# Kernel tuning notes

Measured on AMD Instinct MI355X. Metric: run time of the kernel, lower is better.

Reference implementation:

```python
import jax, jax.numpy as jnp
import numpy as np

S, B, E, H = 2048, 2, 1024, 16
D = E // H  # head_dim = 64


def setup_inputs() -> dict:
    key = jax.random.key(0)
    ks = jax.random.split(key, 5)
    sp = (2.0 / (E + E)) ** 0.5  # xavier-ish scale
    return {
        "x": jax.random.normal(ks[0], (S, B, E), dtype=jnp.float32),
        "wq": jax.random.normal(ks[1], (E, E), dtype=jnp.float32) * sp,
        "bq": jnp.zeros((E,), jnp.float32),
        "wk": jax.random.normal(ks[2], (E, E), dtype=jnp.float32) * sp,
        "bk": jnp.zeros((E,), jnp.float32),
        "wv": jax.random.normal(ks[3], (E, E), dtype=jnp.float32) * sp,
        "bv": jnp.zeros((E,), jnp.float32),
        "wo": jax.random.normal(ks[4], (E, E), dtype=jnp.float32) * sp,
        "bo": jnp.zeros((E,), jnp.float32),
    }


def reference(x, wq, bq, wk, bk, wv, bv, wo, bo):
    # x: (S, B, E), weights in torch Linear convention (out, in)
    scaling = jnp.float32(D ** -0.5)
    q = (jnp.einsum('ibe,fe->ibf', x, wq) + bq) * scaling
    k = jnp.einsum('ibe,fe->ibf', x, wk) + bk
    v = jnp.einsum('ibe,fe->ibf', x, wv) + bv
    q = q.reshape(S, B, H, D)
    k = k.reshape(S, B, H, D)
    v = v.reshape(S, B, H, D)
    # energy: (B, H, S_q, S_k)
    energy = jnp.einsum('ibnf,jbnf->bnij', q, k)
    causal = jnp.triu(jnp.ones((S, S), dtype=bool), k=1)  # True above diagonal
    energy = jnp.where(causal[None, None], -jnp.inf, energy)
    weights = jax.nn.softmax(energy, axis=-1)
    head_ctx = jnp.einsum('bnij,jbnf->ibnf', weights, v)
    context = head_ctx.reshape(S, B, E)
    out = jnp.einsum('ibe,fe->ibf', context, wo) + bo
    return out
```

## Files before the change

kernel.cpp:

```cpp
#include <hip/hip_runtime.h>
#include <hip/hip_bf16.h>
#include <stdint.h>

#define S_LEN 2048
#define BATCH 2
#define EMB   1024
#define NH    16
#define HD    64
#define LOG2E 1.4426950408889634f

typedef __bf16 bf16x8 __attribute__((ext_vector_type(8)));
typedef float  f32x4  __attribute__((ext_vector_type(4)));
typedef unsigned short ushort8 __attribute__((ext_vector_type(8)));

__device__ __forceinline__ unsigned short f2bf(float f) {
  __bf16 h = (__bf16)f;
  return __builtin_bit_cast(unsigned short, h);
}

__device__ __forceinline__ ushort8 cvt8(const float4 a, const float4 b) {
  ushort8 o;
  o[0]=f2bf(a.x); o[1]=f2bf(a.y); o[2]=f2bf(a.z); o[3]=f2bf(a.w);
  o[4]=f2bf(b.x); o[5]=f2bf(b.y); o[6]=f2bf(b.z); o[7]=f2bf(b.w);
  return o;
}

__device__ __forceinline__ uint2 pack4(const f32x4 v) {
  uint2 r;
  r.x = (unsigned)f2bf(v[0]) | ((unsigned)f2bf(v[1]) << 16);
  r.y = (unsigned)f2bf(v[2]) | ((unsigned)f2bf(v[3]) << 16);
  return r;
}

#define GLOAD16(g, l) __builtin_amdgcn_global_load_lds( \
    (const __attribute__((address_space(1))) void*)(g),  \
    (__attribute__((address_space(3))) void*)(l), 16, 0, 0)

__global__ __launch_bounds__(256) void k_cvt(const float* __restrict__ src,
                                             unsigned short* __restrict__ dst,
                                             int n) {
  int i = (blockIdx.x*256 + threadIdx.x)*8;
  if (i >= n) return;
  const float4* s4 = (const float4*)(src + i);
  *(ushort8*)(dst + i) = cvt8(s4[0], s4[1]);
}

__global__ __launch_bounds__(256) void k_cvt_all(
    const float* __restrict__ x,
    const float* __restrict__ wq, const float* __restrict__ wk,
    const float* __restrict__ wv, const float* __restrict__ wo,
    unsigned short* __restrict__ xb, unsigned short* __restrict__ wb,
    unsigned short* __restrict__ wob) {
  const int b = blockIdx.x;
  const float* src;
  unsigned short* dst;
  int off;
  if (b < 2048) { src = x; dst = xb; off = b; }
  else {
    const int t = b - 2048;
    const int z = t >> 9;
    if (z < 3) { src = (z==0) ? wq : ((z==1) ? wk : wv); dst = wb + (size_t)z*EMB*EMB; }
    else       { src = wo; dst = wob; }
    off = t & 511;
  }
  const int i = (off*256 + threadIdx.x)*8;
  const float4* s4 = (const float4*)(src + i);
  *(ushort8*)(dst + i) = cvt8(s4[0], s4[1]);
}

__global__ __launch_bounds__(256) void k_qkv_bb(
    const unsigned short* __restrict__ xb,
    const unsigned short* __restrict__ wb,
    const float* __restrict__ bq, const float* __restrict__ bk,
    const float* __restrict__ bv,
    unsigned short* __restrict__ Qb, unsigned short* __restrict__ Kb,
    unsigned short* __restrict__ Vtb)
{
  __shared__ unsigned short Al[2][128*32];
  __shared__ unsigned short Bl[2][128*32];
  const int tid = threadIdx.x;
  const int lin  = blockIdx.x;
  const int wgid = (lin & 7)*96 + (lin >> 3);
  const int mb   = wgid / 24;
  const int t    = wgid % 24;
  const int z    = t >> 3;
  const int nb   = t & 7;
  const int m0 = mb * 128;
  const int n0 = nb * 128;
  const int w = tid >> 6, lane = tid & 63;
  const int wr = w >> 1, wc = w & 1;
  const int lr = lane & 15, lhi = lane >> 4;
  const unsigned short* wz = wb + (size_t)z * (EMB*EMB);

  const unsigned short* ag[2];
  const unsigned short* bg[2];
  int ub[2];
#pragma unroll
  for (int j=0;j<2;++j) {
    const int c   = j*256 + tid;
    const int row = c >> 2;
    const int col = (c & 3) << 3;
    ag[j] = xb + (size_t)(m0+row)*EMB + col;
    bg[j] = wz + (size_t)(n0+row)*EMB + col;
    ub[j] = (j*256 + (tid & 192)) * 16;
  }

  auto STAGE = [&](int k0, int b2) {
#pragma unroll
    for (int j=0;j<2;++j) {
      GLOAD16(ag[j] + k0, (char*)Al[b2] + ub[j]);
      GLOAD16(bg[j] + k0, (char*)Bl[b2] + ub[j]);
    }
  };

  f32x4 acc[4][4];
#pragma unroll
  for (int m=0;m<4;++m)
#pragma unroll
    for (int n=0;n<4;++n) acc[m][n] = (f32x4){0.f,0.f,0.f,0.f};

  STAGE(0, 0);
  int bbuf = 0;
  for (int k0 = 0; k0 < EMB; k0 += 32) {
    if (k0 + 32 < EMB) {
      STAGE(k0 + 32, bbuf^1);
      asm volatile("s_waitcnt vmcnt(4)" ::: "memory");
    } else {
      asm volatile("s_waitcnt vmcnt(0)" ::: "memory");
    }
    __builtin_amdgcn_s_barrier();

    bf16x8 af[4], bfr[4];
#pragma unroll
    for (int m=0;m<4;++m) af[m]  = *(const bf16x8*)&Al[bbuf][(wr*64 + m*16 + lr)*32 + lhi*8];
#pragma unroll
    for (int n=0;n<4;++n) bfr[n] = *(const bf16x8*)&Bl[bbuf][(wc*64 + n*16 + lr)*32 + lhi*8];
    __builtin_amdgcn_s_setprio(1);
#pragma unroll
    for (int m=0;m<4;++m)
#pragma unroll
      for (int n=0;n<4;++n)
        acc[m][n] = __builtin_amdgcn_mfma_f32_16x16x32_bf16(af[m], bfr[n], acc[m][n], 0,0,0);
    __builtin_amdgcn_s_setprio(0);

    __builtin_amdgcn_s_barrier();
    bbuf ^= 1;
  }

  const float scale = (z==0) ? 0.125f*LOG2E : 1.0f;
  const float* bias = (z==0) ? bq : ((z==1) ? bk : bv);
#pragma unroll
  for (int m=0;m<4;++m)
#pragma unroll
    for (int n=0;n<4;++n)
#pragma unroll
      for (int r=0;r<4;++r) {
        const int rr   = m0 + wr*64 + m*16 + lhi*4 + r;
        const int fcol = n0 + wc*64 + n*16 + lr;
        const float v = (acc[m][n][r] + bias[fcol]) * scale;
        const unsigned short ov = f2bf(v);
        const int i = rr >> 1, bsel = rr & 1;
        const int h = fcol >> 6, d = fcol & 63;
        const int hh = bsel*NH + h;
        if (z == 0)      Qb [((size_t)hh*S_LEN + i)*HD + d] = ov;
        else if (z == 1) Kb [((size_t)hh*S_LEN + i)*HD + d] = ov;
        else             Vtb[((size_t)hh*HD + d)*S_LEN + i] = ov;
      }
}

__global__ __launch_bounds__(256) void k_qkv_bf(
    const unsigned short* __restrict__ xb,
    const float* __restrict__ wq, const float* __restrict__ wk,
    const float* __restrict__ wv,
    const float* __restrict__ bq, const float* __restrict__ bk,
    const float* __restrict__ bv,
    unsigned short* __restrict__ Qb, unsigned short* __restrict__ Kb,
    unsigned short* __restrict__ Vtb)
{
  __shared__ unsigned short Al[128*32];
  __shared__ unsigned short Bl[128*32];
  const int tid = threadIdx.x;
  const int lin  = blockIdx.x;
  const int wgid = (lin & 7)*96 + (lin >> 3);
  const int mb   = wgid / 24;
  const int t    = wgid % 24;
  const int z    = t >> 3;
  const int nb   = t & 7;
  const int m0 = mb * 128;
  const int n0 = nb * 128;
  const int w = tid >> 6, lane = tid & 63;
  const int wr = w >> 1, wc = w & 1;
  const int lr = lane & 15, lhi = lane >> 4;
  const float* wz = (z==0) ? wq : ((z==1) ? wk : wv);

  f32x4 acc[4][4];
#pragma unroll
  for (int m=0;m<4;++m)
#pragma unroll
    for (int n=0;n<4;++n) acc[m][n] = (f32x4){0.f,0.f,0.f,0.f};

  for (int k0 = 0; k0 < EMB; k0 += 32) {
    float4 b0[2], b1[2];
#pragma unroll
    for (int j = 0; j < 2; ++j) {
      const int c   = j*256 + tid;
      const int row = c >> 2;
      const int col = (c & 3) << 3;
      const float* bp = wz + (size_t)(n0+row)*EMB + k0 + col;
      b0[j] = *(const float4*)bp;  b1[j] = *(const float4*)(bp+4);
    }
    __syncthreads();
#pragma unroll
    for (int j = 0; j < 2; ++j) {
      const int c   = j*256 + tid;
      const int row = c >> 2;
      const int col = (c & 3) << 3;
      const int ub  = (j*256 + (tid & 192)) * 16;
      GLOAD16(xb + (size_t)(m0+row)*EMB + k0 + col, (char*)Al + ub);
      *(ushort8*)&Bl[row*32 + col] = cvt8(b0[j], b1[j]);
    }
    __syncthreads();
    bf16x8 af[4], bfr[4];
#pragma unroll
    for (int m=0;m<4;++m) af[m]  = *(const bf16x8*)&Al[(wr*64 + m*16 + lr)*32 + lhi*8];
#pragma unroll
    for (int n=0;n<4;++n) bfr[n] = *(const bf16x8*)&Bl[(wc*64 + n*16 + lr)*32 + lhi*8];
#pragma unroll
    for (int m=0;m<4;++m)
#pragma unroll
      for (int n=0;n<4;++n)
        acc[m][n] = __builtin_amdgcn_mfma_f32_16x16x32_bf16(af[m], bfr[n], acc[m][n], 0,0,0);
  }

  const float scale = (z==0) ? 0.125f*LOG2E : 1.0f;
  const float* bias = (z==0) ? bq : ((z==1) ? bk : bv);
#pragma unroll
  for (int m=0;m<4;++m)
#pragma unroll
    for (int n=0;n<4;++n)
#pragma unroll
      for (int r=0;r<4;++r) {
        const int rr   = m0 + wr*64 + m*16 + lhi*4 + r;
        const int fcol = n0 + wc*64 + n*16 + lr;
        const float v = (acc[m][n][r] + bias[fcol]) * scale;
        const unsigned short ov = f2bf(v);
        const int i = rr >> 1, bsel = rr & 1;
        const int h = fcol >> 6, d = fcol & 63;
        const int hh = bsel*NH + h;
        if (z == 0)      Qb [((size_t)hh*S_LEN + i)*HD + d] = ov;
        else if (z == 1) Kb [((size_t)hh*S_LEN + i)*HD + d] = ov;
        else             Vtb[((size_t)hh*HD + d)*S_LEN + i] = ov;
      }
}

__global__ __launch_bounds__(256) void k_qkv(
    const float* __restrict__ xA, int a_rs, int ishift,
    const float* __restrict__ wq, const float* __restrict__ wk,
    const float* __restrict__ wv,
    const float* __restrict__ bq, const float* __restrict__ bk,
    const float* __restrict__ bv,
    unsigned short* __restrict__ Qb, unsigned short* __restrict__ Kb,
    unsigned short* __restrict__ Vtb)
{
  __shared__ unsigned short Al[128*32];
  __shared__ unsigned short Bl[128*32];
  const int tid = threadIdx.x;
  const int z  = blockIdx.z;
  const int m0 = blockIdx.x * 128;
  const int n0 = blockIdx.y * 128;
  const int w = tid >> 6, lane = tid & 63;
  const int wr = w >> 1, wc = w & 1;
  const int lr = lane & 15, lhi = lane >> 4;
  const float* wz = (z==0) ? wq : ((z==1) ? wk : wv);

  f32x4 acc[4][4];
#pragma unroll
  for (int m=0;m<4;++m)
#pragma unroll
    for (int n=0;n<4;++n) acc[m][n] = (f32x4){0.f,0.f,0.f,0.f};

  for (int k0 = 0; k0 < EMB; k0 += 32) {
    float4 a0[2], a1[2], b0[2], b1[2];
#pragma unroll
    for (int j = 0; j < 2; ++j) {
      const int c   = j*256 + tid;
      const int row = c >> 2;
      const int col = (c & 3) << 3;
      const float* ap = xA + (size_t)(m0+row)*a_rs + k0 + col;
      const float* bp = wz + (size_t)(n0+row)*EMB + k0 + col;
      a0[j] = *(const float4*)ap;  a1[j] = *(const float4*)(ap+4);
      b0[j] = *(const float4*)bp;  b1[j] = *(const float4*)(bp+4);
    }
    __syncthreads();
#pragma unroll
    for (int j = 0; j < 2; ++j) {
      const int c   = j*256 + tid;
      const int row = c >> 2;
      const int col = (c & 3) << 3;
      *(ushort8*)&Al[row*32 + col] = cvt8(a0[j], a1[j]);
      *(ushort8*)&Bl[row*32 + col] = cvt8(b0[j], b1[j]);
    }
    __syncthreads();
    bf16x8 af[4], bfr[4];
#pragma unroll
    for (int m=0;m<4;++m) af[m]  = *(const bf16x8*)&Al[(wr*64 + m*16 + lr)*32 + lhi*8];
#pragma unroll
    for (int n=0;n<4;++n) bfr[n] = *(const bf16x8*)&Bl[(wc*64 + n*16 + lr)*32 + lhi*8];
#pragma unroll
    for (int m=0;m<4;++m)
#pragma unroll
      for (int n=0;n<4;++n)
        acc[m][n] = __builtin_amdgcn_mfma_f32_16x16x32_bf16(af[m], bfr[n], acc[m][n], 0,0,0);
  }

  const float scale = (z==0) ? 0.125f*LOG2E : 1.0f;
  const float* bias = (z==0) ? bq : ((z==1) ? bk : bv);
  const int bmask = (1 << ishift) - 1;
#pragma unroll
  for (int m=0;m<4;++m)
#pragma unroll
    for (int n=0;n<4;++n)
#pragma unroll
      for (int r=0;r<4;++r) {
        const int rr   = m0 + wr*64 + m*16 + lhi*4 + r;
        const int fcol = n0 + wc*64 + n*16 + lr;
        const float v = (acc[m][n][r] + bias[fcol]) * scale;
        const unsigned short ov = f2bf(v);
        const int i = rr >> ishift, bsel = rr & bmask;
        const int h = fcol >> 6, d = fcol & 63;
        const int hh = bsel*NH + h;
        if (z == 0)      Qb [((size_t)hh*S_LEN + i)*HD + d] = ov;
        else if (z == 1) Kb [((size_t)hh*S_LEN + i)*HD + d] = ov;
        else             Vtb[((size_t)hh*HD + d)*S_LEN + i] = ov;
      }
}

__global__ __launch_bounds__(256,4) void k_attn_u(
    const unsigned short* __restrict__ Q,
    const unsigned short* __restrict__ K,
    const unsigned short* __restrict__ Vt,
    unsigned short* __restrict__ ctx, int bshift, int hsh)
{
  __shared__ unsigned short KL[2][64*64];
  __shared__ unsigned short VL[2][64*64];
  __shared__ unsigned short Pl[4][16*64];

  const int tid = threadIdx.x;
  const int w = tid >> 6, lane = tid & 63;
  const int lr = lane & 15, lhi = lane >> 4;

  const int lin = blockIdx.x;
  const int cc  = lin >> hsh;
  const int chunk = (cc < 16) ? cc : (47 - cc);
  const int hh  = lin & ((1 << hsh) - 1);
  const int q0  = chunk*64 + w*16;

  const unsigned short* Qh = Q  + (size_t)hh*S_LEN*HD;
  const unsigned short* Kh = K  + (size_t)hh*S_LEN*HD;
  const unsigned short* Vh = Vt + (size_t)hh*HD*S_LEN;
  char* Pw = (char*)Pl[w];

  const int xm = (lr & 7) << 4;
  int kvb[2];
#pragma unroll
  for (int kf=0;kf<2;++kf) kvb[kf] = lr*128 + ((kf*64 + lhi*16) ^ xm);
  int pwb[4];
#pragma unroll
  for (int kn=0;kn<4;++kn)
    pwb[kn] = lr*128 + ((kn*32 + lhi*8) ^ xm);

  const unsigned short* kga[2];
  const unsigned short* vga[2];
#pragma unroll
  for (int j=0;j<2;++j) {
    const int c   = j*256 + tid;
    const int row = c >> 3;
    const int sb  = (c*16) ^ ((row & 7) << 4);
    const int el  = (sb & 127) >> 1;
    kga[j] = Kh + (size_t)row*HD + el;
    vga[j] = Vh + (size_t)row*S_LEN + el;
  }
  const int ub0 = (tid & 192) * 16;

  bf16x8 qf[2];
#pragma unroll
  for (int kf=0;kf<2;++kf)
    qf[kf] = *(const bf16x8*)&Qh[(size_t)(q0 + lr)*HD + kf*32 + lhi*8];

  f32x4 o[4];
  float rl = 0.f;
#pragma unroll
  for (int dn=0;dn<4;++dn) o[dn] = (f32x4){0.f,0.f,0.f,0.f};

  const int tmax = chunk + 1;

  auto STAGE = [&](int tt, int bb2) {
#pragma unroll
    for (int j=0;j<2;++j) {
      GLOAD16(kga[j] + (size_t)tt*4096, (char*)KL[bb2] + ub0 + j*4096);
      GLOAD16(vga[j] + (size_t)tt*64,   (char*)VL[bb2] + ub0 + j*4096);
    }
  };

  STAGE(0, 0);
  int bb = 0;
  for (int t = 0; t < tmax; ++t) {
    if (t + 1 < tmax) {
      STAGE(t+1, bb^1);
      asm volatile("s_waitcnt vmcnt(4)" ::: "memory");
    } else {
      asm volatile("s_waitcnt vmcnt(0)" ::: "memory");
    }
    __builtin_amdgcn_s_barrier();

    const int kv0 = t*64;
    const char* KB = (const char*)KL[bb];
    const char* VB = (const char*)VL[bb];

    f32x4 st[4];
#pragma unroll
    for (int kn=0;kn<4;++kn) st[kn] = (f32x4){0.f,0.f,0.f,0.f};

    __builtin_amdgcn_s_setprio(1);
#pragma unroll
    for (int kn=0;kn<4;++kn)
#pragma unroll
      for (int kf=0;kf<2;++kf) {
        const bf16x8 kfr = *(const bf16x8*)(KB + kvb[kf] + kn*2048);
        st[kn] = __builtin_amdgcn_mfma_f32_16x16x32_bf16(kfr, qf[kf], st[kn], 0,0,0);
      }
    __builtin_amdgcn_s_setprio(0);

    if (t == tmax-1) {
      const int q = q0 + lr;
#pragma unroll
      for (int kn=0;kn<4;++kn)
#pragma unroll
        for (int r=0;r<4;++r) {
          const int k = kv0 + kn*16 + lhi*4 + r;
          if (k > q) st[kn][r] = -1.0e30f;
        }
    }

#pragma unroll
    for (int kn=0;kn<4;++kn)
#pragma unroll
      for (int r=0;r<4;++r) {
        const float p = exp2f(st[kn][r]);
        st[kn][r] = p;
        rl += p;
      }

#pragma unroll
    for (int kn=0;kn<4;++kn)
      *(uint2*)(Pw + pwb[kn]) = pack4(st[kn]);

#pragma unroll
    for (int ks=0;ks<2;++ks) {
      const bf16x8 pfr = *(const bf16x8*)(Pw + kvb[ks]);
      __builtin_amdgcn_s_setprio(1);
#pragma unroll
      for (int dn=0;dn<4;++dn) {
        const bf16x8 vf = *(const bf16x8*)(VB + kvb[ks] + dn*2048);
        o[dn] = __builtin_amdgcn_mfma_f32_16x16x32_bf16(vf, pfr, o[dn], 0,0,0);
      }
      __builtin_amdgcn_s_setprio(0);
    }

    __builtin_amdgcn_s_barrier();
    bb ^= 1;
  }

  rl += __shfl_xor(rl, 16);
  rl += __shfl_xor(rl, 32);
  const int h = hh & (NH-1);
  const int badd = hh >> 4;
  const float inv = 1.0f / rl;
  const int q = q0 + lr;
  const size_t trow = ((size_t)q << bshift) + badd;
#pragma unroll
  for (int dn=0;dn<4;++dn) {
    f32x4 ov;
#pragma unroll
    for (int r=0;r<4;++r) ov[r] = o[dn][r]*inv;
    *(uint2*)&ctx[trow*EMB + h*HD + dn*16 + lhi*4] = pack4(ov);
  }
}

__global__ __launch_bounds__(256) void k_oproj_bf(
    const unsigned short* __restrict__ ctxA,
    const unsigned short* __restrict__ wob,
    const float* __restrict__ bo,
    float* __restrict__ out)
{
  __shared__ unsigned short Al[2][128*32];
  __shared__ unsigned short Bl[2][128*32];
  const int tid = threadIdx.x;
  const int m0 = blockIdx.x * 128;
  const int n0 = blockIdx.y * 128;
  const int w = tid >> 6, lane = tid & 63;
  const int wr = w >> 1, wc = w & 1;
  const int lr = lane & 15, lhi = lane >> 4;

  const unsigned short* ag[2];
  const unsigned short* bg[2];
  int ub[2];
#pragma unroll
  for (int j=0;j<2;++j) {
    const int c   = j*256 + tid;
    const int row = c >> 2;
    const int col = (c & 3) << 3;
    ag[j] = ctxA + (size_t)(m0+row)*EMB + col;
    bg[j] = wob  + (size_t)(n0+row)*EMB + col;
    ub[j] = (j*256 + (tid & 192)) * 16;
  }

  auto STAGE = [&](int k0, int b2) {
#pragma unroll
    for (int j=0;j<2;++j) {
      GLOAD16(ag[j] + k0, (char*)Al[b2] + ub[j]);
      GLOAD16(bg[j] + k0, (char*)Bl[b2] + ub[j]);
    }
  };

  f32x4 acc[4][4];
#pragma unroll
  for (int m=0;m<4;++m)
#pragma unroll
    for (int n=0;n<4;++n) acc[m][n] = (f32x4){0.f,0.f,0.f,0.f};

  STAGE(0, 0);
  int bbuf = 0;
  for (int k0 = 0; k0 < EMB; k0 += 32) {
    if (k0 + 32 < EMB) {
      STAGE(k0 + 32, bbuf^1);
      asm volatile("s_waitcnt vmcnt(4)" ::: "memory");
    } else {
      asm volatile("s_waitcnt vmcnt(0)" ::: "memory");
    }
    __builtin_amdgcn_s_barrier();

    bf16x8 af[4], bfr[4];
#pragma unroll
    for (int m=0;m<4;++m) af[m]  = *(const bf16x8*)&Al[bbuf][(wr*64 + m*16 + lr)*32 + lhi*8];
#pragma unroll
    for (int n=0;n<4;++n) bfr[n] = *(const bf16x8*)&Bl[bbuf][(wc*64 + n*16 + lr)*32 + lhi*8];
    __builtin_amdgcn_s_setprio(1);
#pragma unroll
    for (int m=0;m<4;++m)
#pragma unroll
      for (int n=0;n<4;++n)
        acc[m][n] = __builtin_amdgcn_mfma_f32_16x16x32_bf16(af[m], bfr[n], acc[m][n], 0,0,0);
    __builtin_amdgcn_s_setprio(0);

    __builtin_amdgcn_s_barrier();
    bbuf ^= 1;
  }

#pragma unroll
  for (int m=0;m<4;++m)
#pragma unroll
    for (int n=0;n<4;++n)
#pragma unroll
      for (int r=0;r<4;++r) {
        const int rr   = m0 + wr*64 + m*16 + lhi*4 + r;
        const int fcol = n0 + wc*64 + n*16 + lr;
        out[(size_t)rr*EMB + fcol] = acc[m][n][r] + bo[fcol];
      }
}

__global__ __launch_bounds__(256) void k_oproj(
    const unsigned short* __restrict__ ctxA,
    const float* __restrict__ wo,
    const float* __restrict__ bo,
    float* __restrict__ outb, int orm)
{
  __shared__ unsigned short Al[128*32];
  __shared__ unsigned short Bl[128*32];
  const int tid = threadIdx.x;
  const int m0 = blockIdx.x * 128;
  const int n0 = blockIdx.y * 128;
  const int w = tid >> 6, lane = tid & 63;
  const int wr = w >> 1, wc = w & 1;
  const int lr = lane & 15, lhi = lane >> 4;

  f32x4 acc[4][4];
#pragma unroll
  for (int m=0;m<4;++m)
#pragma unroll
    for (int n=0;n<4;++n) acc[m][n] = (f32x4){0.f,0.f,0.f,0.f};

  for (int k0 = 0; k0 < EMB; k0 += 32) {
    float4 b0[2], b1[2];
#pragma unroll
    for (int j = 0; j < 2; ++j) {
      const int c   = j*256 + tid;
      const int row = c >> 2;
      const int col = (c & 3) << 3;
      const float* bp = wo + (size_t)(n0+row)*EMB + k0 + col;
      b0[j] = *(const float4*)bp;  b1[j] = *(const float4*)(bp+4);
    }
    __syncthreads();
#pragma unroll
    for (int j = 0; j < 2; ++j) {
      const int c   = j*256 + tid;
      const int row = c >> 2;
      const int col = (c & 3) << 3;
      const int ub  = (j*256 + (tid & 192)) * 16;
      GLOAD16(ctxA + (size_t)(m0+row)*EMB + k0 + col, (char*)Al + ub);
      *(ushort8*)&Bl[row*32 + col] = cvt8(b0[j], b1[j]);
    }
    __syncthreads();
    bf16x8 af[4], bfr[4];
#pragma unroll
    for (int m=0;m<4;++m) af[m]  = *(const bf16x8*)&Al[(wr*64 + m*16 + lr)*32 + lhi*8];
#pragma unroll
    for (int n=0;n<4;++n) bfr[n] = *(const bf16x8*)&Bl[(wc*64 + n*16 + lr)*32 + lhi*8];
#pragma unroll
    for (int m=0;m<4;++m)
#pragma unroll
      for (int n=0;n<4;++n)
        acc[m][n] = __builtin_amdgcn_mfma_f32_16x16x32_bf16(af[m], bfr[n], acc[m][n], 0,0,0);
  }

#pragma unroll
  for (int m=0;m<4;++m)
#pragma unroll
    for (int n=0;n<4;++n)
#pragma unroll
      for (int r=0;r<4;++r) {
        const int rr   = m0 + wr*64 + m*16 + lhi*4 + r;
        const int fcol = n0 + wc*64 + n*16 + lr;
        outb[(size_t)rr*orm*EMB + fcol] = acc[m][n][r] + bo[fcol];
      }
}

extern "C" void kernel_launch(void* const* d_in, const int* in_sizes, int n_in,
                              void* d_out, int out_size, void* d_ws, size_t ws_size,
                              hipStream_t stream) {
  const float* x  = (const float*)d_in[0];
  const float* wq = (const float*)d_in[1];
  const float* bq = (const float*)d_in[2];
  const float* wk = (const float*)d_in[3];
  const float* bk = (const float*)d_in[4];
  const float* wv = (const float*)d_in[5];
  const float* bv = (const float*)d_in[6];
  const float* wo = (const float*)d_in[7];
  const float* bo = (const float*)d_in[8];
  float* out = (float*)d_out;

  char* ws = (char*)d_ws;
  const size_t MB = (size_t)1 << 20;

  if (ws_size >= 40*MB) {
    unsigned short* Q   = (unsigned short*)(ws + 0*MB);
    unsigned short* K   = (unsigned short*)(ws + 8*MB);
    unsigned short* Vt  = (unsigned short*)(ws + 16*MB);
    unsigned short* wb  = (unsigned short*)(ws + 24*MB);
    unsigned short* xb  = (unsigned short*)(ws + 30*MB);
    unsigned short* wob = (unsigned short*)(ws + 38*MB);
    unsigned short* cx  = (unsigned short*)(ws + 24*MB);

    k_cvt_all<<<4096, 256, 0, stream>>>(x, wq, wk, wv, wo, xb, wb, wob);
    k_qkv_bb<<<768, 256, 0, stream>>>(xb, wb, bq,bk,bv, Q, K, Vt);
    k_attn_u<<<1024, 256, 0, stream>>>(Q, K, Vt, cx, 1, 5);
    k_oproj_bf<<<dim3(32,8), 256, 0, stream>>>(cx, wob, bo, out);
  } else if (ws_size >= 38*MB) {
    unsigned short* Q   = (unsigned short*)(ws + 0*MB);
    unsigned short* K   = (unsigned short*)(ws + 8*MB);
    unsigned short* Vt  = (unsigned short*)(ws + 16*MB);
    unsigned short* wb  = (unsigned short*)(ws + 24*MB);
    unsigned short* xb  = (unsigned short*)(ws + 30*MB);
    unsigned short* cx  = (unsigned short*)(ws + 24*MB);
    unsigned short* wob = Vt;

    k_cvt_all<<<3584, 256, 0, stream>>>(x, wq, wk, wv, wo, xb, wb, (unsigned short*)0);
    k_qkv_bb<<<768, 256, 0, stream>>>(xb, wb, bq,bk,bv, Q, K, Vt);
    k_attn_u<<<1024, 256, 0, stream>>>(Q, K, Vt, cx, 1, 5);
    k_cvt<<<512, 256, 0, stream>>>(wo, wob, EMB*EMB);
    k_oproj_bf<<<dim3(32,8), 256, 0, stream>>>(cx, wob, bo, out);
  } else if (ws_size >= 32*MB) {
    unsigned short* Q   = (unsigned short*)(ws + 0*MB);
    unsigned short* K   = (unsigned short*)(ws + 8*MB);
    unsigned short* Vt  = (unsigned short*)(ws + 16*MB);
    unsigned short* cx  = (unsigned short*)(ws + 24*MB);
    unsigned short* xb  = cx;
    unsigned short* wob = Vt;

    k_cvt<<<2048, 256, 0, stream>>>(x, xb, (S_LEN*BATCH)*EMB);
    k_qkv_bf<<<768, 256, 0, stream>>>(xb, wq,wk,wv, bq,bk,bv, Q, K, Vt);
    k_attn_u<<<1024, 256, 0, stream>>>(Q, K, Vt, cx, 1, 5);
    k_cvt<<<512, 256, 0, stream>>>(wo, wob, EMB*EMB);
    k_oproj_bf<<<dim3(32,8), 256, 0, stream>>>(cx, wob, bo, out);
  } else {
    unsigned short* Q  = (unsigned short*)(ws + 0*MB);
    unsigned short* K  = (unsigned short*)(ws + 4*MB);
    unsigned short* Vt = (unsigned short*)(ws + 8*MB);
    unsigned short* cx = (unsigned short*)(ws + 12*MB);
    for (int b = 0; b < 2; ++b) {
      k_qkv<<<dim3(16,8,3), 256, 0, stream>>>(x + b*EMB, 2*EMB, 0,
                                              wq,wk,wv, bq,bk,bv, Q,K,Vt);
      k_attn_u<<<512, 256, 0, stream>>>(Q, K, Vt, cx, 0, 4);
      k_oproj<<<dim3(16,8), 256, 0, stream>>>(cx, wo, bo, out + b*EMB, 2);
    }
  }
}
```

Baseline: 115.6 us.

## Swizzle GEMM LDS tiles and load V directly from global in attention

In the QKV-projection and output-projection GEMMs, the global-to-LDS staging is remapped with an XOR swizzle over pairs of rows, and the fragment reads use matching swizzled offsets. The goal is to remove LDS bank conflicts on the 16-byte fragment reads. In the attention kernel, V is no longer staged through LDS. Each wave reads its V fragments straight from global memory into registers every iteration, which halves LDS traffic and footprint but puts uncoalesced, possibly uncached global loads on the critical path without prefetch.

```diff
diff --git a/kernel.cpp b/kernel.cpp
--- a/kernel.cpp
+++ b/kernel.cpp
@@ -97,11 +97,13 @@
   int ub[2];
 #pragma unroll
   for (int j=0;j<2;++j) {
-    const int c   = j*256 + tid;
-    const int row = c >> 2;
-    const int col = (c & 3) << 3;
-    ag[j] = xb + (size_t)(m0+row)*EMB + col;
-    bg[j] = wz + (size_t)(n0+row)*EMB + col;
+    const int c    = j*256 + tid;
+    const int line = c >> 3;
+    const int sp   = (c & 7) ^ (line & 7);
+    const int row  = line*2 + (sp >> 2);
+    const int q    = sp & 3;
+    ag[j] = xb + (size_t)(m0+row)*EMB + q*8;
+    bg[j] = wz + (size_t)(n0+row)*EMB + q*8;
     ub[j] = (j*256 + (tid & 192)) * 16;
   }
 
@@ -112,6 +114,11 @@
       GLOAD16(bg[j] + k0, (char*)Bl[b2] + ub[j]);
     }
   };
+
+  const int asl  = (((lr & 1) << 2) + lhi) ^ (lr >> 1);
+  const int rb   = (lr >> 1)*128 + asl*16;
+  const int abase = wr*4096 + rb;
+  const int bbase = wc*4096 + rb;
 
   f32x4 acc[4][4];
 #pragma unroll
@@ -132,9 +139,9 @@
 
     bf16x8 af[4], bfr[4];
 #pragma unroll
-    for (int m=0;m<4;++m) af[m]  = *(const bf16x8*)&Al[bbuf][(wr*64 + m*16 + lr)*32 + lhi*8];
-#pragma unroll
-    for (int n=0;n<4;++n) bfr[n] = *(const bf16x8*)&Bl[bbuf][(wc*64 + n*16 + lr)*32 + lhi*8];
+    for (int m=0;m<4;++m) af[m]  = *(const bf16x8*)((char*)Al[bbuf] + abase + m*1024);
+#pragma unroll
+    for (int n=0;n<4;++n) bfr[n] = *(const bf16x8*)((char*)Bl[bbuf] + bbase + n*1024);
     __builtin_amdgcn_s_setprio(1);
 #pragma unroll
     for (int m=0;m<4;++m)
@@ -342,7 +349,6 @@
     unsigned short* __restrict__ ctx, int bshift, int hsh)
 {
   __shared__ unsigned short KL[2][64*64];
-  __shared__ unsigned short VL[2][64*64];
   __shared__ unsigned short Pl[4][16*64];
 
   const int tid = threadIdx.x;
@@ -370,7 +376,6 @@
     pwb[kn] = lr*128 + ((kn*32 + lhi*8) ^ xm);
 
   const unsigned short* kga[2];
-  const unsigned short* vga[2];
 #pragma unroll
   for (int j=0;j<2;++j) {
     const int c   = j*256 + tid;
@@ -378,9 +383,9 @@
     const int sb  = (c*16) ^ ((row & 7) << 4);
     const int el  = (sb & 127) >> 1;
     kga[j] = Kh + (size_t)row*HD + el;
-    vga[j] = Vh + (size_t)row*S_LEN + el;
   }
   const int ub0 = (tid & 192) * 16;
+  const unsigned short* vgb = Vh + (size_t)lr*S_LEN + lhi*8;
 
   bf16x8 qf[2];
 #pragma unroll
@@ -396,10 +401,8 @@
 
   auto STAGE = [&](int tt, int bb2) {
 #pragma unroll
-    for (int j=0;j<2;++j) {
+    for (int j=0;j<2;++j)
       GLOAD16(kga[j] + (size_t)tt*4096, (char*)KL[bb2] + ub0 + j*4096);
-      GLOAD16(vga[j] + (size_t)tt*64,   (char*)VL[bb2] + ub0 + j*4096);
-    }
   };
 
   STAGE(0, 0);
@@ -407,7 +410,7 @@
   for (int t = 0; t < tmax; ++t) {
     if (t + 1 < tmax) {
       STAGE(t+1, bb^1);
-      asm volatile("s_waitcnt vmcnt(4)" ::: "memory");
+      asm volatile("s_waitcnt vmcnt(2)" ::: "memory");
     } else {
       asm volatile("s_waitcnt vmcnt(0)" ::: "memory");
     }
@@ -415,7 +418,13 @@
 
     const int kv0 = t*64;
     const char* KB = (const char*)KL[bb];
-    const char* VB = (const char*)VL[bb];
+
+    bf16x8 vf[2][4];
+#pragma unroll
+    for (int ks=0;ks<2;++ks)
+#pragma unroll
+      for (int dn=0;dn<4;++dn)
+        vf[ks][dn] = *(const bf16x8*)(vgb + dn*32768 + ks*32 + kv0);
 
     f32x4 st[4];
 #pragma unroll
@@ -460,10 +469,8 @@
       const bf16x8 pfr = *(const bf16x8*)(Pw + kvb[ks]);
       __builtin_amdgcn_s_setprio(1);
 #pragma unroll
-      for (int dn=0;dn<4;++dn) {
-        const bf16x8 vf = *(const bf16x8*)(VB + kvb[ks] + dn*2048);
-        o[dn] = __builtin_amdgcn_mfma_f32_16x16x32_bf16(vf, pfr, o[dn], 0,0,0);
-      }
+      for (int dn=0;dn<4;++dn)
+        o[dn] = __builtin_amdgcn_mfma_f32_16x16x32_bf16(vf[ks][dn], pfr, o[dn], 0,0,0);
       __builtin_amdgcn_s_setprio(0);
     }
 
@@ -507,11 +514,13 @@
   int ub[2];
 #pragma unroll
   for (int j=0;j<2;++j) {
-    const int c   = j*256 + tid;
-    const int row = c >> 2;
-    const int col = (c & 3) << 3;
-    ag[j] = ctxA + (size_t)(m0+row)*EMB + col;
-    bg[j] = wob  + (size_t)(n0+row)*EMB + col;
+    const int c    = j*256 + tid;
+    const int line = c >> 3;
+    const int sp   = (c & 7) ^ (line & 7);
+    const int row  = line*2 + (sp >> 2);
+    const int q    = sp & 3;
+    ag[j] = ctxA + (size_t)(m0+row)*EMB + q*8;
+    bg[j] = wob  + (size_t)(n0+row)*EMB + q*8;
     ub[j] = (j*256 + (tid & 192)) * 16;
   }
 
@@ -522,6 +531,11 @@
       GLOAD16(bg[j] + k0, (char*)Bl[b2] + ub[j]);
     }
   };
+
+  const int asl  = (((lr & 1) << 2) + lhi) ^ (lr >> 1);
+  const int rb   = (lr >> 1)*128 + asl*16;
+  const int abase = wr*4096 + rb;
+  const int bbase = wc*4096 + rb;
 
   f32x4 acc[4][4];
 #pragma unroll
@@ -542,9 +556,9 @@
 
     bf16x8 af[4], bfr[4];
 #pragma unroll
-    for (int m=0;m<4;++m) af[m]  = *(const bf16x8*)&Al[bbuf][(wr*64 + m*16 + lr)*32 + lhi*8];
-#pragma unroll
-    for (int n=0;n<4;++n) bfr[n] = *(const bf16x8*)&Bl[bbuf][(wc*64 + n*16 + lr)*32 + lhi*8];
+    for (int m=0;m<4;++m) af[m]  = *(const bf16x8*)((char*)Al[bbuf] + abase + m*1024);
+#pragma unroll
+    for (int n=0;n<4;++n) bfr[n] = *(const bf16x8*)((char*)Bl[bbuf] + bbase + n*1024);
     __builtin_amdgcn_s_setprio(1);
 #pragma unroll
     for (int m=0;m<4;++m)
```

Result: slower. 143.7 us (+24.3%).
